# Kernel optimization log

Measured on AMD Instinct MI355X. Metric: run time of the kernel, lower is better.

## Reference

```python
import jax, jax.numpy as jnp
import numpy as np

FUTURE_K = 16
NEG_BIG = -1e9  # matches masked softmax semantics (invalid slots get exactly 0 weight in fp32)


def setup_inputs() -> dict:
    key = jax.random.key(0)
    hidden_states = jax.random.normal(key, (2, 4096, 1024), dtype=jnp.float32)
    return {"hidden_states": hidden_states}


def reference(hidden_states) -> jnp.ndarray:
    # Windowed future attention: for each position t, attend over the next
    # FUTURE_K hidden states (t+1 .. t+k), masked at the sequence end.
    B, S, H = hidden_states.shape
    k = FUTURE_K
    # pad on the right so every window is full-length
    x_padded = jnp.pad(hidden_states, ((0, 0), (0, k), (0, 0)))  # (B, S+k, H)
    t = jnp.arange(S)
    gidx = t[:, None] + 1 + jnp.arange(k)[None, :]               # (S, k) global indices
    windows = x_padded[:, gidx]                                   # (B, S, k, H)
    valid = gidx < S                                              # (S, k)
    # per-window dot-product scores, masked softmax over window slots
    scores = jnp.einsum('bth,btjh->btj', hidden_states, windows)  # (B, S, k)
    scores = jnp.where(valid[None], scores, NEG_BIG)
    weights = jax.nn.softmax(scores, axis=-1)
    # rows with no valid future (last positions) -> zero summary (torch nan_to_num)
    weights = jnp.where(valid[None], weights, 0.0)
    summary = jnp.einsum('btj,btjh->bth', weights, windows)       # (B, S, H)
    return summary
```

## Files before the change

kernel.cpp:

```cpp
#include <hip/hip_runtime.h>


namespace {
constexpr int kB   = 2;
constexpr int kS   = 4096;
constexpr int kH   = 1024;
constexpr int kK   = 16;
constexpr int kTPW = 2;
constexpr int kFR  = kH / (64 * 4);
constexpr int kRows = kK + kTPW - 1;
constexpr int kXCD = 8;
constexpr int kWavesPerBlk = 4;
constexpr int kBlocks = kB * kS / (kTPW * kWavesPerBlk);
}

__global__ __launch_bounds__(256, 4)
void future_encoder_kernel(const float* __restrict__ x, float* __restrict__ out) {
  const int lane = (int)(threadIdx.x & 63);
  const int wib  = (int)(threadIdx.x >> 6);

  const int vb   = (int)(blockIdx.x % kXCD) * (kBlocks / kXCD) + (int)(blockIdx.x / kXCD);
  const int wave = vb * kWavesPerBlk + wib;
  const int t0g  = wave * kTPW;
  const int b    = t0g / kS;
  const int tl0  = t0g % kS;
  const float* __restrict__ xb = x   + (size_t)b * kS * kH;
  float* __restrict__       ob = out + (size_t)b * kS * kH;
  const int col = lane * 4;

  float4 xt[kTPW][kFR];
#pragma unroll
  for (int tt = 0; tt < kTPW; ++tt)
#pragma unroll
    for (int p = 0; p < kFR; ++p)
      xt[tt][p] = *(const float4*)(xb + (size_t)(tl0 + tt) * kH + p * 256 + col);

  float m[kTPW], s[kTPW];
  float4 acc[kTPW][kFR];
#pragma unroll
  for (int tt = 0; tt < kTPW; ++tt) {
    m[tt] = -1e30f;
    s[tt] = 0.f;
#pragma unroll
    for (int p = 0; p < kFR; ++p) acc[tt][p] = make_float4(0.f, 0.f, 0.f, 0.f);
  }

#pragma unroll
  for (int j = 0; j < kRows; ++j) {
    const int rr = tl0 + 1 + j;
    const int r  = (rr < kS) ? rr : (kS - 1);

    float4 w[kFR];
#pragma unroll
    for (int p = 0; p < kFR; ++p)
      w[p] = *(const float4*)(xb + (size_t)r * kH + p * 256 + col);

    float sc[kTPW];
#pragma unroll
    for (int tt = 0; tt < kTPW; ++tt) {
      const int d = 1 + j - tt;
      if (d >= 1 && d <= kK) {
        float a0 = 0.f, a1 = 0.f;
#pragma unroll
        for (int p = 0; p < kFR; ++p) {
          a0 = fmaf(xt[tt][p].x, w[p].x, a0);
          a1 = fmaf(xt[tt][p].y, w[p].y, a1);
          a0 = fmaf(xt[tt][p].z, w[p].z, a0);
          a1 = fmaf(xt[tt][p].w, w[p].w, a1);
        }
        sc[tt] = a0 + a1;
      } else {
        sc[tt] = 0.f;
      }
    }

#pragma unroll
    for (int off = 32; off >= 1; off >>= 1) {
      float other[kTPW];
#pragma unroll
      for (int tt = 0; tt < kTPW; ++tt) other[tt] = __shfl_xor(sc[tt], off, 64);
#pragma unroll
      for (int tt = 0; tt < kTPW; ++tt) sc[tt] += other[tt];
    }

    if (rr < kS) {
#pragma unroll
      for (int tt = 0; tt < kTPW; ++tt) {
        const int d = 1 + j - tt;
        if (d >= 1 && d <= kK) {
          const float v = sc[tt];
          if (v <= m[tt]) {
            const float p2 = __expf(v - m[tt]);
            s[tt] += p2;
#pragma unroll
            for (int p = 0; p < kFR; ++p) {
              acc[tt][p].x = fmaf(p2, w[p].x, acc[tt][p].x);
              acc[tt][p].y = fmaf(p2, w[p].y, acc[tt][p].y);
              acc[tt][p].z = fmaf(p2, w[p].z, acc[tt][p].z);
              acc[tt][p].w = fmaf(p2, w[p].w, acc[tt][p].w);
            }
          } else {
            const float r2 = __expf(m[tt] - v);
            m[tt] = v;
            s[tt] = fmaf(s[tt], r2, 1.f);
#pragma unroll
            for (int p = 0; p < kFR; ++p) {
              acc[tt][p].x = fmaf(acc[tt][p].x, r2, w[p].x);
              acc[tt][p].y = fmaf(acc[tt][p].y, r2, w[p].y);
              acc[tt][p].z = fmaf(acc[tt][p].z, r2, w[p].z);
              acc[tt][p].w = fmaf(acc[tt][p].w, r2, w[p].w);
            }
          }
        }
      }
    }
  }

#pragma unroll
  for (int tt = 0; tt < kTPW; ++tt) {
    const float inv = (s[tt] > 0.f) ? (1.f / s[tt]) : 0.f;
#pragma unroll
    for (int p = 0; p < kFR; ++p) {
      float4 o;
      o.x = acc[tt][p].x * inv;
      o.y = acc[tt][p].y * inv;
      o.z = acc[tt][p].z * inv;
      o.w = acc[tt][p].w * inv;
      *(float4*)(ob + (size_t)(tl0 + tt) * kH + p * 256 + col) = o;
    }
  }
}

extern "C" void kernel_launch(void* const* d_in, const int* in_sizes, int n_in,
                              void* d_out, int out_size, void* d_ws, size_t ws_size,
                              hipStream_t stream) {
  const float* x = (const float*)d_in[0];
  float* out = (float*)d_out;
  hipLaunchKernelGGL(future_encoder_kernel, dim3(kBlocks), dim3(256), 0, stream,
                     x, out);
}
```

Baseline: 26.27 us.

## Stage shared window rows in double-buffered LDS across a 32-token block

Each 512-thread block now covers 32 consecutive tokens (8 waves × 4 tokens). The 48 needed rows are streamed in chunks of 8 into a double-buffered LDS tile using global_load_lds, and every wave reads its window rows and its own query rows from LDS. The aim is to cut redundant global/L2 reads of overlapping windows, since each row is fetched once per block instead of once per wave. In exchange it adds block-wide barriers on every chunk, 64KB of LDS, and more register pressure from 4 tokens per wave. Waves whose window does not overlap a chunk sit idle, which reduces occupancy.

```diff
diff --git a/kernel.cpp b/kernel.cpp
--- a/kernel.cpp
+++ b/kernel.cpp
@@ -6,36 +6,34 @@
 constexpr int kS   = 4096;
 constexpr int kH   = 1024;
 constexpr int kK   = 16;
-constexpr int kTPW = 2;
-constexpr int kFR  = kH / (64 * 4);
-constexpr int kRows = kK + kTPW - 1;
-constexpr int kXCD = 8;
-constexpr int kWavesPerBlk = 4;
-constexpr int kBlocks = kB * kS / (kTPW * kWavesPerBlk);
+constexpr int kWaves = 8;
+constexpr int kTPW   = 4;
+constexpr int kTPB   = kWaves * kTPW;
+constexpr int kRows  = kTPB + kK;
+constexpr int kCH    = 8;
+constexpr int kChunks = kRows / kCH;
+constexpr int kFR    = kH / (64 * 4);
+constexpr int kBlocks = kB * kS / kTPB;
+constexpr int kXCD   = 8;
 }
 
-__global__ __launch_bounds__(256, 4)
+__global__ __launch_bounds__(512, 2)
 void future_encoder_kernel(const float* __restrict__ x, float* __restrict__ out) {
+  __shared__ float lds[2][kCH][kH];
   const int lane = (int)(threadIdx.x & 63);
-  const int wib  = (int)(threadIdx.x >> 6);
+  const int wid  = (int)(threadIdx.x >> 6);
 
-  const int vb   = (int)(blockIdx.x % kXCD) * (kBlocks / kXCD) + (int)(blockIdx.x / kXCD);
-  const int wave = vb * kWavesPerBlk + wib;
-  const int t0g  = wave * kTPW;
-  const int b    = t0g / kS;
-  const int tl0  = t0g % kS;
+  const int vb  = (int)(blockIdx.x % kXCD) * (kBlocks / kXCD) + (int)(blockIdx.x / kXCD);
+  const int t0g = vb * kTPB;
+  const int b   = t0g / kS;
+  const int t0  = t0g % kS;
   const float* __restrict__ xb = x   + (size_t)b * kS * kH;
   float* __restrict__       ob = out + (size_t)b * kS * kH;
   const int col = lane * 4;
+  const int tw  = kTPW * wid;
 
   float4 xt[kTPW][kFR];
-#pragma unroll
-  for (int tt = 0; tt < kTPW; ++tt)
-#pragma unroll
-    for (int p = 0; p < kFR; ++p)
-      xt[tt][p] = *(const float4*)(xb + (size_t)(tl0 + tt) * kH + p * 256 + col);
-
-  float m[kTPW], s[kTPW];
+  float  m[kTPW], s[kTPW];
   float4 acc[kTPW][kFR];
 #pragma unroll
   for (int tt = 0; tt < kTPW; ++tt) {
@@ -45,80 +43,112 @@
     for (int p = 0; p < kFR; ++p) acc[tt][p] = make_float4(0.f, 0.f, 0.f, 0.f);
   }
 
+  {
+    const int gr = t0 + wid;
+    const float* g = xb + (size_t)gr * kH + col;
+    float* l = &lds[0][wid][0];
 #pragma unroll
-  for (int j = 0; j < kRows; ++j) {
-    const int rr = tl0 + 1 + j;
-    const int r  = (rr < kS) ? rr : (kS - 1);
+    for (int seg = 0; seg < 4; ++seg)
+      __builtin_amdgcn_global_load_lds(
+          (const __attribute__((address_space(1))) void*)(g + seg * 256),
+          (__attribute__((address_space(3))) void*)(l + seg * 256), 16, 0, 0);
+  }
+  __syncthreads();
 
-    float4 w[kFR];
 #pragma unroll
-    for (int p = 0; p < kFR; ++p)
-      w[p] = *(const float4*)(xb + (size_t)r * kH + p * 256 + col);
+  for (int c = 0; c < kChunks; ++c) {
+    if (c + 1 < kChunks) {
+      const int ri = (c + 1) * kCH + wid;
+      int gr = t0 + ri; if (gr > kS - 1) gr = kS - 1;
+      const float* g = xb + (size_t)gr * kH + col;
+      float* l = &lds[(c + 1) & 1][wid][0];
+#pragma unroll
+      for (int seg = 0; seg < 4; ++seg)
+        __builtin_amdgcn_global_load_lds(
+            (const __attribute__((address_space(1))) void*)(g + seg * 256),
+            (__attribute__((address_space(3))) void*)(l + seg * 256), 16, 0, 0);
+    }
 
-    float sc[kTPW];
+    if ((wid >> 1) == c) {
 #pragma unroll
-    for (int tt = 0; tt < kTPW; ++tt) {
-      const int d = 1 + j - tt;
-      if (d >= 1 && d <= kK) {
-        float a0 = 0.f, a1 = 0.f;
+      for (int tt = 0; tt < kTPW; ++tt)
 #pragma unroll
-        for (int p = 0; p < kFR; ++p) {
-          a0 = fmaf(xt[tt][p].x, w[p].x, a0);
-          a1 = fmaf(xt[tt][p].y, w[p].y, a1);
-          a0 = fmaf(xt[tt][p].z, w[p].z, a0);
-          a1 = fmaf(xt[tt][p].w, w[p].w, a1);
-        }
-        sc[tt] = a0 + a1;
-      } else {
-        sc[tt] = 0.f;
-      }
+        for (int p = 0; p < kFR; ++p)
+          xt[tt][p] = *(const float4*)&lds[c & 1][4 * (wid & 1) + tt][p * 256 + col];
     }
 
 #pragma unroll
-    for (int off = 32; off >= 1; off >>= 1) {
-      float other[kTPW];
+    for (int jr = 0; jr < kCH; ++jr) {
+      const int ri  = c * kCH + jr;
+      const int rel = ri - tw;
+      if (rel >= 1 && rel <= kTPW - 1 + kK && (t0 + ri) < kS) {
+        float4 w[kFR];
 #pragma unroll
-      for (int tt = 0; tt < kTPW; ++tt) other[tt] = __shfl_xor(sc[tt], off, 64);
+        for (int p = 0; p < kFR; ++p)
+          w[p] = *(const float4*)&lds[c & 1][jr][p * 256 + col];
+
+        float sc[kTPW];
 #pragma unroll
-      for (int tt = 0; tt < kTPW; ++tt) sc[tt] += other[tt];
-    }
+        for (int tt = 0; tt < kTPW; ++tt) {
+          float a0 = 0.f, a1 = 0.f;
+#pragma unroll
+          for (int p = 0; p < kFR; ++p) {
+            a0 = fmaf(xt[tt][p].x, w[p].x, a0);
+            a1 = fmaf(xt[tt][p].y, w[p].y, a1);
+            a0 = fmaf(xt[tt][p].z, w[p].z, a0);
+            a1 = fmaf(xt[tt][p].w, w[p].w, a1);
+          }
+          sc[tt] = a0 + a1;
+        }
 
-    if (rr < kS) {
 #pragma unroll
-      for (int tt = 0; tt < kTPW; ++tt) {
-        const int d = 1 + j - tt;
-        if (d >= 1 && d <= kK) {
-          const float v = sc[tt];
-          if (v <= m[tt]) {
-            const float p2 = __expf(v - m[tt]);
-            s[tt] += p2;
+        for (int off = 32; off >= 1; off >>= 1) {
+          float other[kTPW];
 #pragma unroll
-            for (int p = 0; p < kFR; ++p) {
-              acc[tt][p].x = fmaf(p2, w[p].x, acc[tt][p].x);
-              acc[tt][p].y = fmaf(p2, w[p].y, acc[tt][p].y);
-              acc[tt][p].z = fmaf(p2, w[p].z, acc[tt][p].z);
-              acc[tt][p].w = fmaf(p2, w[p].w, acc[tt][p].w);
-            }
-          } else {
-            const float r2 = __expf(m[tt] - v);
-            m[tt] = v;
-            s[tt] = fmaf(s[tt], r2, 1.f);
+          for (int tt = 0; tt < kTPW; ++tt) other[tt] = __shfl_xor(sc[tt], off, 64);
 #pragma unroll
-            for (int p = 0; p < kFR; ++p) {
-              acc[tt][p].x = fmaf(acc[tt][p].x, r2, w[p].x);
-              acc[tt][p].y = fmaf(acc[tt][p].y, r2, w[p].y);
-              acc[tt][p].z = fmaf(acc[tt][p].z, r2, w[p].z);
-              acc[tt][p].w = fmaf(acc[tt][p].w, r2, w[p].w);
+          for (int tt = 0; tt < kTPW; ++tt) sc[tt] += other[tt];
+        }
+
+#pragma unroll
+        for (int tt = 0; tt < kTPW; ++tt) {
+          const int d = rel - tt;
+          if (d >= 1 && d <= kK) {
+            const float v = sc[tt];
+            if (v <= m[tt]) {
+              const float p2 = __expf(v - m[tt]);
+              s[tt] += p2;
+#pragma unroll
+              for (int p = 0; p < kFR; ++p) {
+                acc[tt][p].x = fmaf(p2, w[p].x, acc[tt][p].x);
+                acc[tt][p].y = fmaf(p2, w[p].y, acc[tt][p].y);
+                acc[tt][p].z = fmaf(p2, w[p].z, acc[tt][p].z);
+                acc[tt][p].w = fmaf(p2, w[p].w, acc[tt][p].w);
+              }
+            } else {
+              const float r2 = __expf(m[tt] - v);
+              m[tt] = v;
+              s[tt] = fmaf(s[tt], r2, 1.f);
+#pragma unroll
+              for (int p = 0; p < kFR; ++p) {
+                acc[tt][p].x = fmaf(acc[tt][p].x, r2, w[p].x);
+                acc[tt][p].y = fmaf(acc[tt][p].y, r2, w[p].y);
+                acc[tt][p].z = fmaf(acc[tt][p].z, r2, w[p].z);
+                acc[tt][p].w = fmaf(acc[tt][p].w, r2, w[p].w);
+              }
             }
           }
         }
       }
     }
+
+    __syncthreads();
   }
 
 #pragma unroll
   for (int tt = 0; tt < kTPW; ++tt) {
     const float inv = (s[tt] > 0.f) ? (1.f / s[tt]) : 0.f;
+    const int t = t0 + tw + tt;
 #pragma unroll
     for (int p = 0; p < kFR; ++p) {
       float4 o;
@@ -126,7 +156,7 @@
       o.y = acc[tt][p].y * inv;
       o.z = acc[tt][p].z * inv;
       o.w = acc[tt][p].w * inv;
-      *(float4*)(ob + (size_t)(tl0 + tt) * kH + p * 256 + col) = o;
+      *(float4*)(ob + (size_t)t * kH + p * 256 + col) = o;
     }
   }
 }
@@ -136,6 +166,6 @@
                               hipStream_t stream) {
   const float* x = (const float*)d_in[0];
   float* out = (float*)d_out;
-  hipLaunchKernelGGL(future_encoder_kernel, dim3(kBlocks), dim3(256), 0, stream,
+  hipLaunchKernelGGL(future_encoder_kernel, dim3(kBlocks), dim3(512), 0, stream,
                      x, out);
 }
```

Result: slower. 52.67 us (+100.5%).
